# Optimization experiments

Measured on AMD Instinct MI355X. Metric: run time of the kernel, lower is better.

Reference implementation:

```python
import jax, jax.numpy as jnp
import numpy as np

N, E = 50000, 500000          # nodes, edges
IN_DIM, HID, OUT = 512, 256, 64  # hidden_dims = [in_dim, num_hidden, out_dim]


def setup_inputs() -> dict:
    key = jax.random.key(0)
    ks = jax.random.split(key, 6)
    features = jax.random.normal(ks[0], (N, IN_DIM), jnp.float32)
    edge_index = jax.random.randint(ks[1], (2, E), 0, N, jnp.int32)  # [src; dst]
    s1 = 1.0 / np.sqrt(IN_DIM)
    s2 = 1.0 / np.sqrt(HID)
    # torch.nn.Linear convention: weight shape (out, in), y = x @ W.T
    W1 = jax.random.uniform(ks[2], (HID, IN_DIM), jnp.float32, -s1, s1)
    W2 = jax.random.uniform(ks[3], (OUT, HID), jnp.float32, -s2, s2)
    att_src = jax.random.normal(ks[4], (HID,), jnp.float32) * 0.1
    att_dst = jax.random.normal(ks[5], (HID,), jnp.float32) * 0.1
    return dict(features=features, W1=W1, W2=W2,
                att_src=att_src, att_dst=att_dst, edge_index=edge_index)


def _gat_propagate(h, a_src, a_dst, src, dst, n):
    """STAGATE GATConv propagate: sigmoid attention logits + PyG segment softmax
    over destination nodes, then scatter-sum of weighted source features."""
    a = jax.nn.sigmoid(a_src[src] + a_dst[dst])          # [E] edge logits
    mx = jax.ops.segment_max(a, dst, num_segments=n)     # [N] per-dest max
    mx = jnp.where(jnp.isfinite(mx), mx, 0.0)            # empty segments -> 0
    e = jnp.exp(a - mx[dst])                             # [E]
    denom = jax.ops.segment_sum(e, dst, num_segments=n)  # [N]
    w = e / (denom[dst] + 1e-16)                         # [E] softmax weights
    return jax.ops.segment_sum(h[src] * w[:, None], dst, num_segments=n)


def reference(features, W1, W2, att_src, att_dst, edge_index):
    src, dst = edge_index[0], edge_index[1]
    n = features.shape[0]
    # conv1: attention=True (heads=1, concat=False)
    h1p = features @ W1.T                 # [N, HID]
    a_src = h1p @ att_src                 # [N] node-level alpha_src
    a_dst = h1p @ att_dst                 # [N] node-level alpha_dst
    h1 = jax.nn.elu(_gat_propagate(h1p, a_src, a_dst, src, dst, n))
    # conv2: attention=False -> linear only
    h2 = h1 @ W2.T                        # [N, OUT]
    # conv3: weight tied to W2.T, tied_attention = conv1's node alphas
    h3p = h2 @ W2                         # [N, HID]
    h3 = jax.nn.elu(_gat_propagate(h3p, a_src, a_dst, src, dst, n))
    # conv4: attention=False, weight tied to W1.T
    h4 = h3 @ W1                          # [N, IN_DIM]
    return h2, h4
```

## Files before the change

kernel.cpp:

```cpp
#include <hip/hip_runtime.h>
#include <hip/hip_bf16.h>

typedef unsigned short u16;
typedef unsigned int   u32;

#define N_NODES 50000
#define N_EDGES 500000
#define IN_DIM  512
#define HID     256
#define OUT_DIM 64

typedef __bf16 bf16x8 __attribute__((ext_vector_type(8)));
typedef float  f32x4  __attribute__((ext_vector_type(4)));

#define GLOBAL_AS __attribute__((address_space(1)))
#define LDS_AS    __attribute__((address_space(3)))

__device__ __forceinline__ float bf2f(u16 u) {
  union { u32 i; float f; } x; x.i = ((u32)u) << 16; return x.f;
}
__device__ __forceinline__ u16 f2bf(float f) {
  union { float f; u32 i; } x; x.f = f;
  u32 r = x.i + 0x7FFFu + ((x.i >> 16) & 1u);
  return (u16)(r >> 16);
}
__device__ __forceinline__ float lo2f(u32 w) {
  union { u32 i; float f; } x; x.i = w << 16; return x.f;
}
__device__ __forceinline__ float hi2f(u32 w) {
  union { u32 i; float f; } x; x.i = w & 0xFFFF0000u; return x.f;
}

__global__ void detect_dtype(const u32* __restrict__ feat, int* __restrict__ flag) {
  __shared__ int s[256];
  int t = threadIdx.x;
  int hits = 0;
  for (int i = t; i < 1024; i += 256) {
    u32 e = (feat[i] >> 7) & 0xFF;
    hits += (e >= 100 && e <= 140) ? 1 : 0;
  }
  s[t] = hits;
  __syncthreads();
  for (int o = 128; o > 0; o >>= 1) {
    if (t < o) s[t] += s[t + o];
    __syncthreads();
  }
  if (t == 0) *flag = (s[0] > 716) ? 1 : 0;
}

__global__ void cvt8(const void* __restrict__ src, u16* __restrict__ dst, int n8,
                     const int* __restrict__ flag) {
  int i = blockIdx.x * 256 + threadIdx.x;
  if (i >= n8) return;
  if (*flag) {
    ((uint4*)dst)[i] = ((const uint4*)src)[i];
  } else {
    const float4* s4 = (const float4*)src;
    float4 a = s4[2 * i], b = s4[2 * i + 1];
    uint4 o;
    o.x = (u32)f2bf(a.x) | ((u32)f2bf(a.y) << 16);
    o.y = (u32)f2bf(a.z) | ((u32)f2bf(a.w) << 16);
    o.z = (u32)f2bf(b.x) | ((u32)f2bf(b.y) << 16);
    o.w = (u32)f2bf(b.z) | ((u32)f2bf(b.w) << 16);
    ((uint4*)dst)[i] = o;
  }
}

__global__ void transpose_bf16(const u16* __restrict__ src, u16* __restrict__ dst,
                               int R, int C) {
  int i = blockIdx.x * 256 + threadIdx.x;
  if (i < R * C) {
    int r = i / C, c = i - r * C;
    dst[c * R + r] = src[i];
  }
}

__device__ __forceinline__ void glds16(const u16* g, __bf16* l) {
  __builtin_amdgcn_global_load_lds((const GLOBAL_AS u32*)g, (LDS_AS u32*)l, 16, 0, 0);
}

template <int MODE>
__global__ __launch_bounds__(256) void gemm128(const u16* __restrict__ A,
                                               const u16* __restrict__ B,
                                               u16* __restrict__ Cb,
                                               void* __restrict__ outbase,
                                               size_t out_off,
                                               const int* __restrict__ flag,
                                               int M, int N, int K) {
  __shared__ __bf16 As[128 * 32];
  __shared__ __bf16 Bs[128 * 32];

  const int tid  = threadIdx.x;
  const int wave = tid >> 6;
  const int lane = tid & 63;
  const int m0   = blockIdx.x * 128;
  const int n0   = blockIdx.y * 128;
  const int wm   = (wave >> 1) * 64;
  const int wn   = (wave & 1) * 64;
  const int quad = lane >> 4;
  const int l16  = lane & 15;

  const int r_in  = lane >> 2;
  const int s_log = (lane & 3) ^ ((lane >> 3) & 3);
  const int q0 = wave, q1 = wave + 4;
  int ar0 = m0 + q0 * 16 + r_in; if (ar0 >= M) ar0 = M - 1;
  int ar1 = m0 + q1 * 16 + r_in; if (ar1 >= M) ar1 = M - 1;
  const u16* ap0 = A + (size_t)ar0 * K + s_log * 8;
  const u16* ap1 = A + (size_t)ar1 * K + s_log * 8;
  const u16* bp0 = B + (size_t)(n0 + q0 * 16 + r_in) * K + s_log * 8;
  const u16* bp1 = B + (size_t)(n0 + q1 * 16 + r_in) * K + s_log * 8;

  f32x4 acc[4][4];
#pragma unroll
  for (int i = 0; i < 4; ++i)
#pragma unroll
    for (int j = 0; j < 4; ++j) acc[i][j] = (f32x4)0.f;

  const int swz = (l16 >> 1) & 3;

  for (int k0 = 0; k0 < K; k0 += 32) {
    __syncthreads();
    glds16(ap0 + k0, As + q0 * 512);
    glds16(ap1 + k0, As + q1 * 512);
    glds16(bp0 + k0, Bs + q0 * 512);
    glds16(bp1 + k0, Bs + q1 * 512);
    __syncthreads();

    bf16x8 af[4], bfr[4];
#pragma unroll
    for (int mi = 0; mi < 4; ++mi)
      af[mi] = *(const bf16x8*)&As[(wm + mi * 16 + l16) * 32 + ((quad ^ swz) * 8)];
#pragma unroll
    for (int ni = 0; ni < 4; ++ni)
      bfr[ni] = *(const bf16x8*)&Bs[(wn + ni * 16 + l16) * 32 + ((quad ^ swz) * 8)];
#pragma unroll
    for (int mi = 0; mi < 4; ++mi)
#pragma unroll
      for (int ni = 0; ni < 4; ++ni)
        acc[mi][ni] = __builtin_amdgcn_mfma_f32_16x16x32_bf16(
            af[mi], bfr[ni], acc[mi][ni], 0, 0, 0);
  }

  const int out_bf = (MODE == 1) ? *flag : 0;
#pragma unroll
  for (int mi = 0; mi < 4; ++mi)
#pragma unroll
    for (int ni = 0; ni < 4; ++ni)
#pragma unroll
      for (int r = 0; r < 4; ++r) {
        int gr = m0 + wm + mi * 16 + quad * 4 + r;
        int gc = n0 + wn + ni * 16 + l16;
        if (gr < M) {
          float  v   = acc[mi][ni][r];
          size_t idx = (size_t)gr * N + gc;
          if (MODE == 0) {
            Cb[idx] = f2bf(v);
          } else {
            if (out_bf) ((u16*)outbase)[out_off + idx] = f2bf(v);
            else        ((float*)outbase)[out_off + idx] = v;
          }
        }
      }
}

template <int MODE>
__global__ __launch_bounds__(256) void gemm_nt(const u16* __restrict__ A,
                                               const u16* __restrict__ B,
                                               float* __restrict__ Cf,
                                               void* __restrict__ outbase,
                                               size_t out_off,
                                               u16* __restrict__ Cb,
                                               const int* __restrict__ flag,
                                               int M, int N, int K) {
  __shared__ __bf16 As[64 * 48];
  __shared__ __bf16 Bs[64 * 48];

  const int tid  = threadIdx.x;
  const int m0   = blockIdx.x * 64;
  const int n0   = blockIdx.y * 64;
  const int wave = tid >> 6;
  const int lane = tid & 63;
  const int wm   = (wave >> 1) * 32;
  const int wn   = (wave & 1) * 32;
  const int quad = lane >> 4;
  const int l16  = lane & 15;

  const int srow = tid >> 2;
  const int sseg = (tid & 3) * 8;
  int arow = m0 + srow;
  if (arow >= M) arow = M - 1;
  const size_t a_base = (size_t)arow * K + sseg;
  const size_t b_base = (size_t)(n0 + srow) * K + sseg;

  f32x4 acc[2][2];
#pragma unroll
  for (int i = 0; i < 2; ++i)
#pragma unroll
    for (int j = 0; j < 2; ++j) acc[i][j] = (f32x4)0.f;

  for (int k0 = 0; k0 < K; k0 += 32) {
    uint4 av = *(const uint4*)(A + a_base + k0);
    uint4 bv = *(const uint4*)(B + b_base + k0);
    __syncthreads();
    *(uint4*)(&As[srow * 48 + sseg]) = av;
    *(uint4*)(&Bs[srow * 48 + sseg]) = bv;
    __syncthreads();

    bf16x8 af[2], bfr[2];
#pragma unroll
    for (int mi = 0; mi < 2; ++mi)
      af[mi] = *(const bf16x8*)(&As[(wm + mi * 16 + l16) * 48 + quad * 8]);
#pragma unroll
    for (int ni = 0; ni < 2; ++ni)
      bfr[ni] = *(const bf16x8*)(&Bs[(wn + ni * 16 + l16) * 48 + quad * 8]);
#pragma unroll
    for (int mi = 0; mi < 2; ++mi)
#pragma unroll
      for (int ni = 0; ni < 2; ++ni)
        acc[mi][ni] = __builtin_amdgcn_mfma_f32_16x16x32_bf16(
            af[mi], bfr[ni], acc[mi][ni], 0, 0, 0);
  }

  const int out_bf = *flag;
#pragma unroll
  for (int mi = 0; mi < 2; ++mi)
#pragma unroll
    for (int ni = 0; ni < 2; ++ni)
#pragma unroll
      for (int r = 0; r < 4; ++r) {
        int gr = m0 + wm + mi * 16 + quad * 4 + r;
        int gc = n0 + wn + ni * 16 + l16;
        if (gr < M) {
          float  v   = acc[mi][ni][r];
          size_t idx = (size_t)gr * N + gc;
          if (out_bf) ((u16*)outbase)[out_off + idx] = f2bf(v);
          else        ((float*)outbase)[out_off + idx] = v;
          if (MODE == 2) Cb[idx] = f2bf(v);
        }
      }
  (void)Cf;
}

__global__ __launch_bounds__(256) void attn_dots(const u16* __restrict__ h1,
                                                 const u16* __restrict__ atts,
                                                 const u16* __restrict__ attd,
                                                 float* __restrict__ a_s,
                                                 float* __restrict__ a_d) {
  __shared__ __align__(16) float ss[HID];
  __shared__ __align__(16) float sd[HID];
  int t = threadIdx.x;
  ss[t] = bf2f(atts[t]);
  sd[t] = bf2f(attd[t]);
  __syncthreads();
  int row  = blockIdx.x * 4 + (t >> 6);
  int lane = t & 63;
  ushort4 h = ((const ushort4*)(h1 + (size_t)row * HID))[lane];
  float4  s = ((const float4*)ss)[lane];
  float4  d = ((const float4*)sd)[lane];
  float hx = bf2f(h.x), hy = bf2f(h.y), hz = bf2f(h.z), hw = bf2f(h.w);
  float vs = hx * s.x + hy * s.y + hz * s.z + hw * s.w;
  float vd = hx * d.x + hy * d.y + hz * d.z + hw * d.w;
#pragma unroll
  for (int off = 32; off > 0; off >>= 1) {
    vs += __shfl_down(vs, off);
    vd += __shfl_down(vd, off);
  }
  if (lane == 0) {
    a_s[row] = vs;
    a_d[row] = vd;
  }
}

__global__ void hist_kernel(const int* __restrict__ dst, int* __restrict__ counts) {
  int e = blockIdx.x * 256 + threadIdx.x;
  if (e < N_EDGES) atomicAdd(&counts[dst[e]], 1);
}

__global__ void block_sum(const int* __restrict__ counts, int n,
                          int* __restrict__ bsums) {
  __shared__ int s[256];
  int i = blockIdx.x * 256 + threadIdx.x;
  s[threadIdx.x] = (i < n) ? counts[i] : 0;
  __syncthreads();
  for (int off = 128; off > 0; off >>= 1) {
    if (threadIdx.x < off) s[threadIdx.x] += s[threadIdx.x + off];
    __syncthreads();
  }
  if (threadIdx.x == 0) bsums[blockIdx.x] = s[0];
}

__global__ void scan_bsums(const int* __restrict__ bsums, int nb,
                           int* __restrict__ boffs) {
  __shared__ int s[256];
  int t = threadIdx.x;
  int v = (t < nb) ? bsums[t] : 0;
  s[t] = v;
  __syncthreads();
  for (int off = 1; off < 256; off <<= 1) {
    int add = (t >= off) ? s[t - off] : 0;
    __syncthreads();
    s[t] += add;
    __syncthreads();
  }
  boffs[t] = s[t] - v;
}

__global__ void scan_final(const int* __restrict__ counts,
                           const int* __restrict__ boffs, int n,
                           int* __restrict__ offsets, int* __restrict__ cursor) {
  __shared__ int s[256];
  int t = threadIdx.x;
  int i = blockIdx.x * 256 + t;
  int v = (i < n) ? counts[i] : 0;
  s[t] = v;
  __syncthreads();
  for (int off = 1; off < 256; off <<= 1) {
    int add = (t >= off) ? s[t - off] : 0;
    __syncthreads();
    s[t] += add;
    __syncthreads();
  }
  int excl = boffs[blockIdx.x] + s[t] - v;
  if (i < n) {
    offsets[i] = excl;
    cursor[i]  = excl;
  }
  if (i == n - 1) offsets[n] = excl + v;
}

__global__ void edge_scatter(const int* __restrict__ src, const int* __restrict__ dst,
                             const float* __restrict__ a_s, const float* __restrict__ a_d,
                             float* __restrict__ denom, int* __restrict__ cursor,
                             int* __restrict__ csr_src, float* __restrict__ csr_e) {
  int e = blockIdx.x * 256 + threadIdx.x;
  if (e >= N_EDGES) return;
  int s = src[e], d = dst[e];
  float x  = a_s[s] + a_d[d];
  float a  = 1.f / (1.f + expf(-x));
  float ev = expf(a);
  atomicAdd(&denom[d], ev);
  int pos = atomicAdd(&cursor[d], 1);
  csr_src[pos] = s;
  csr_e[pos]   = ev;
}

__global__ __launch_bounds__(256) void propagate_elu8(
    const int* __restrict__ offs, const int* __restrict__ csr_src,
    const float* __restrict__ csr_e, const float* __restrict__ denom,
    const u16* __restrict__ feat, u16* __restrict__ out) {
  const int sub  = threadIdx.x >> 5;
  const int lane = threadIdx.x & 31;
  const int nd   = blockIdx.x * 8 + sub;
  const int col  = lane * 8;
  const int beg = offs[nd], end = offs[nd + 1];
  float a[8];
#pragma unroll
  for (int j = 0; j < 8; ++j) a[j] = 0.f;
  for (int e = beg; e < end; ++e) {
    int   s  = csr_src[e];
    float ev = csr_e[e];
    uint4 w = *(const uint4*)(feat + (size_t)s * HID + col);
    a[0] += ev * lo2f(w.x); a[1] += ev * hi2f(w.x);
    a[2] += ev * lo2f(w.y); a[3] += ev * hi2f(w.y);
    a[4] += ev * lo2f(w.z); a[5] += ev * hi2f(w.z);
    a[6] += ev * lo2f(w.w); a[7] += ev * hi2f(w.w);
  }
  float dn = 1.f / (denom[nd] + 1e-16f);
  uint4 o;
  u32 p[4];
#pragma unroll
  for (int j = 0; j < 4; ++j) {
    float r0 = a[2 * j] * dn;
    float r1 = a[2 * j + 1] * dn;
    r0 = (r0 > 0.f) ? r0 : expm1f(r0);
    r1 = (r1 > 0.f) ? r1 : expm1f(r1);
    p[j] = (u32)f2bf(r0) | ((u32)f2bf(r1) << 16);
  }
  o.x = p[0]; o.y = p[1]; o.z = p[2]; o.w = p[3];
  *(uint4*)(out + (size_t)nd * HID + col) = o;
}

extern "C" void kernel_launch(void* const* d_in, const int* in_sizes, int n_in,
                              void* d_out, int out_size, void* d_ws, size_t ws_size,
                              hipStream_t stream) {
  const void* X    = d_in[0];
  const void* W1   = d_in[1];
  const void* W2   = d_in[2];
  const void* atts = d_in[3];
  const void* attd = d_in[4];
  const int*  eidx = (const int*)d_in[5];
  const int*  esrc = eidx;
  const int*  edst = eidx + N_EDGES;

  char*  ws  = (char*)d_ws;
  size_t off = 0;
  auto alloc = [&](size_t bytes) -> void* {
    void* p = ws + off;
    off += (bytes + 255) & ~(size_t)255;
    return p;
  };
  u16*   Xb     = (u16*)alloc((size_t)N_NODES * IN_DIM * 2);
  u16*   W1b    = (u16*)alloc((size_t)HID * IN_DIM * 2);
  u16*   W2b    = (u16*)alloc((size_t)OUT_DIM * HID * 2);
  u16*   attsb  = (u16*)alloc(HID * 2);
  u16*   attdb  = (u16*)alloc(HID * 2);
  u16*   W1T    = (u16*)alloc((size_t)IN_DIM * HID * 2);
  u16*   W2T    = (u16*)alloc((size_t)HID * OUT_DIM * 2);
  u16*   feat   = (u16*)alloc((size_t)N_NODES * HID * 2);
  u16*   h1     = (u16*)alloc((size_t)N_NODES * HID * 2);
  u16*   h2b    = (u16*)alloc((size_t)N_NODES * OUT_DIM * 2);
  float* a_s    = (float*)alloc(N_NODES * 4);
  float* a_d    = (float*)alloc(N_NODES * 4);
  float* denom  = (float*)alloc(N_NODES * 4);
  int*   counts = (int*)alloc(N_NODES * 4);
  int*   offsets= (int*)alloc((N_NODES + 1) * 4);
  int*   cursor = (int*)alloc(N_NODES * 4);
  int*   bsums  = (int*)alloc(1024 * 4);
  int*   boffs  = (int*)alloc(1024 * 4);
  int*   csrsrc = (int*)alloc((size_t)N_EDGES * 4);
  float* csre   = (float*)alloc((size_t)N_EDGES * 4);
  int*   flag   = (int*)alloc(256);
  (void)ws_size; (void)in_sizes; (void)n_in; (void)out_size;

  size_t zero_bytes = (size_t)((char*)offsets - (char*)denom);
  hipMemsetAsync(denom, 0, zero_bytes, stream);

  detect_dtype<<<1, 256, 0, stream>>>((const u32*)X, flag);

  cvt8<<<(N_NODES * IN_DIM / 8 + 255) / 256, 256, 0, stream>>>(X, Xb, N_NODES * IN_DIM / 8, flag);
  cvt8<<<(HID * IN_DIM / 8 + 255) / 256, 256, 0, stream>>>(W1, W1b, HID * IN_DIM / 8, flag);
  cvt8<<<(OUT_DIM * HID / 8 + 255) / 256, 256, 0, stream>>>(W2, W2b, OUT_DIM * HID / 8, flag);
  cvt8<<<1, 256, 0, stream>>>(atts, attsb, HID / 8, flag);
  cvt8<<<1, 256, 0, stream>>>(attd, attdb, HID / 8, flag);

  transpose_bf16<<<(HID * IN_DIM + 255) / 256, 256, 0, stream>>>(W1b, W1T, HID, IN_DIM);
  transpose_bf16<<<(OUT_DIM * HID + 255) / 256, 256, 0, stream>>>(W2b, W2T, OUT_DIM, HID);

  const int MB128 = (N_NODES + 127) / 128;
  const int MB64  = (N_NODES + 63) / 64;
  gemm128<0><<<dim3(MB128, HID / 128), 256, 0, stream>>>(Xb, W1b, feat, nullptr, 0, flag,
                                                         N_NODES, HID, IN_DIM);
  attn_dots<<<N_NODES / 4, 256, 0, stream>>>(feat, attsb, attdb, a_s, a_d);

  const int NB = (N_NODES + 255) / 256;
  hist_kernel<<<(N_EDGES + 255) / 256, 256, 0, stream>>>(edst, counts);
  block_sum<<<NB, 256, 0, stream>>>(counts, N_NODES, bsums);
  scan_bsums<<<1, 256, 0, stream>>>(bsums, NB, boffs);
  scan_final<<<NB, 256, 0, stream>>>(counts, boffs, N_NODES, offsets, cursor);
  edge_scatter<<<(N_EDGES + 255) / 256, 256, 0, stream>>>(esrc, edst, a_s, a_d,
                                                          denom, cursor, csrsrc, csre);
  propagate_elu8<<<N_NODES / 8, 256, 0, stream>>>(offsets, csrsrc, csre, denom, feat, h1);
  gemm_nt<2><<<dim3(MB64, 1), 256, 0, stream>>>(h1, W2b, nullptr, d_out, 0, h2b, flag,
                                                N_NODES, OUT_DIM, HID);
  gemm128<0><<<dim3(MB128, HID / 128), 256, 0, stream>>>(h2b, W2T, feat, nullptr, 0, flag,
                                                         N_NODES, HID, OUT_DIM);
  propagate_elu8<<<N_NODES / 8, 256, 0, stream>>>(offsets, csrsrc, csre, denom, feat, h1);
  gemm128<1><<<dim3(MB128, IN_DIM / 128), 256, 0, stream>>>(h1, W1T, nullptr, d_out,
                                                            (size_t)N_NODES * OUT_DIM, flag,
                                                            N_NODES, IN_DIM, HID);
}
```

Before: 491.5 us.

## Reorder conv3 propagate before W2 projection, fuse attention dots and conversions

```diff
diff --git a/kernel.cpp b/kernel.cpp
--- a/kernel.cpp
+++ b/kernel.cpp
@@ -48,30 +48,48 @@
   if (t == 0) *flag = (s[0] > 716) ? 1 : 0;
 }
 
-__global__ void cvt8(const void* __restrict__ src, u16* __restrict__ dst, int n8,
-                     const int* __restrict__ flag) {
+__global__ void cvt8_cond(const void* __restrict__ src, u16* __restrict__ dst,
+                          int n8, const int* __restrict__ flag) {
+  if (*flag) return;
   int i = blockIdx.x * 256 + threadIdx.x;
   if (i >= n8) return;
-  if (*flag) {
-    ((uint4*)dst)[i] = ((const uint4*)src)[i];
-  } else {
-    const float4* s4 = (const float4*)src;
-    float4 a = s4[2 * i], b = s4[2 * i + 1];
-    uint4 o;
-    o.x = (u32)f2bf(a.x) | ((u32)f2bf(a.y) << 16);
-    o.y = (u32)f2bf(a.z) | ((u32)f2bf(a.w) << 16);
-    o.z = (u32)f2bf(b.x) | ((u32)f2bf(b.y) << 16);
-    o.w = (u32)f2bf(b.z) | ((u32)f2bf(b.w) << 16);
-    ((uint4*)dst)[i] = o;
-  }
-}
-
-__global__ void transpose_bf16(const u16* __restrict__ src, u16* __restrict__ dst,
-                               int R, int C) {
+  const float4* s4 = (const float4*)src;
+  float4 a = s4[2 * i], b = s4[2 * i + 1];
+  uint4 o;
+  o.x = (u32)f2bf(a.x) | ((u32)f2bf(a.y) << 16);
+  o.y = (u32)f2bf(a.z) | ((u32)f2bf(a.w) << 16);
+  o.z = (u32)f2bf(b.x) | ((u32)f2bf(b.y) << 16);
+  o.w = (u32)f2bf(b.z) | ((u32)f2bf(b.w) << 16);
+  ((uint4*)dst)[i] = o;
+}
+
+__global__ void prep(const void* __restrict__ W1r, const void* __restrict__ W2r,
+                     const void* __restrict__ atsr, const void* __restrict__ atdr,
+                     u16* __restrict__ W1b, u16* __restrict__ W2b,
+                     u16* __restrict__ attsb, u16* __restrict__ attdb,
+                     u16* __restrict__ W1T, u16* __restrict__ W2T,
+                     const int* __restrict__ flag) {
+  const int fv = *flag;
   int i = blockIdx.x * 256 + threadIdx.x;
-  if (i < R * C) {
-    int r = i / C, c = i - r * C;
-    dst[c * R + r] = src[i];
+  int stride = gridDim.x * 256;
+  const int NW1 = HID * IN_DIM;
+  const int NW2 = OUT_DIM * HID;
+  for (int j = i; j < NW1; j += stride) {
+    u16 v = fv ? ((const u16*)W1r)[j] : f2bf(((const float*)W1r)[j]);
+    W1b[j] = v;
+    int r = j >> 9, c = j & 511;
+    W1T[c * HID + r] = v;
+  }
+  for (int j = i; j < NW2; j += stride) {
+    u16 v = fv ? ((const u16*)W2r)[j] : f2bf(((const float*)W2r)[j]);
+    W2b[j] = v;
+    int r = j >> 8, c = j & 255;
+    W2T[c * OUT_DIM + r] = v;
+  }
+  if (blockIdx.x == 0 && threadIdx.x < HID) {
+    int t = threadIdx.x;
+    attsb[t] = fv ? ((const u16*)atsr)[t] : f2bf(((const float*)atsr)[t]);
+    attdb[t] = fv ? ((const u16*)atdr)[t] : f2bf(((const float*)atdr)[t]);
   }
 }
 
@@ -81,14 +99,24 @@
 
 template <int MODE>
 __global__ __launch_bounds__(256) void gemm128(const u16* __restrict__ A,
+                                               const u16* __restrict__ Aalt,
                                                const u16* __restrict__ B,
                                                u16* __restrict__ Cb,
                                                void* __restrict__ outbase,
                                                size_t out_off,
+                                               const u16* __restrict__ attsb,
+                                               const u16* __restrict__ attdb,
+                                               float* __restrict__ a_s,
+                                               float* __restrict__ a_d,
                                                const int* __restrict__ flag,
                                                int M, int N, int K) {
   __shared__ __bf16 As[128 * 32];
   __shared__ __bf16 Bs[128 * 32];
+  __shared__ float as_l[128];
+  __shared__ float ad_l[128];
+
+  const int fv = *flag;
+  if (Aalt && fv) A = Aalt;
 
   const int tid  = threadIdx.x;
   const int wave = tid >> 6;
@@ -100,6 +128,11 @@
   const int quad = lane >> 4;
   const int l16  = lane & 15;
 
+  if (MODE == 3 && tid < 128) {
+    as_l[tid] = bf2f(attsb[n0 + tid]);
+    ad_l[tid] = bf2f(attdb[n0 + tid]);
+  }
+
   const int r_in  = lane >> 2;
   const int s_log = (lane & 3) ^ ((lane >> 3) & 3);
   const int q0 = wave, q1 = wave + 4;
@@ -141,7 +174,32 @@
             af[mi], bfr[ni], acc[mi][ni], 0, 0, 0);
   }
 
-  const int out_bf = (MODE == 1) ? *flag : 0;
+  if (MODE == 3) {
+    __syncthreads();
+#pragma unroll
+    for (int mi = 0; mi < 4; ++mi)
+#pragma unroll
+      for (int r = 0; r < 4; ++r) {
+        float ps = 0.f, pd = 0.f;
+#pragma unroll
+        for (int ni = 0; ni < 4; ++ni) {
+          int c = wn + ni * 16 + l16;
+          ps += acc[mi][ni][r] * as_l[c];
+          pd += acc[mi][ni][r] * ad_l[c];
+        }
+#pragma unroll
+        for (int o = 1; o < 16; o <<= 1) {
+          ps += __shfl_xor(ps, o);
+          pd += __shfl_xor(pd, o);
+        }
+        int gr = m0 + wm + mi * 16 + quad * 4 + r;
+        if (l16 == 0 && gr < M) {
+          atomicAdd(&a_s[gr], ps);
+          atomicAdd(&a_d[gr], pd);
+        }
+      }
+  }
+
 #pragma unroll
   for (int mi = 0; mi < 4; ++mi)
 #pragma unroll
@@ -153,22 +211,22 @@
         if (gr < M) {
           float  v   = acc[mi][ni][r];
           size_t idx = (size_t)gr * N + gc;
-          if (MODE == 0) {
+          if (MODE == 1) {
+            if (fv) ((u16*)outbase)[out_off + idx] = f2bf(v);
+            else    ((float*)outbase)[out_off + idx] = v;
+          } else if (MODE == 2) {
+            v = (v > 0.f) ? v : expm1f(v);
             Cb[idx] = f2bf(v);
           } else {
-            if (out_bf) ((u16*)outbase)[out_off + idx] = f2bf(v);
-            else        ((float*)outbase)[out_off + idx] = v;
+            Cb[idx] = f2bf(v);
           }
         }
       }
 }
 
-template <int MODE>
-__global__ __launch_bounds__(256) void gemm_nt(const u16* __restrict__ A,
+__global__ __launch_bounds__(256) void gemm_h2(const u16* __restrict__ A,
                                                const u16* __restrict__ B,
-                                               float* __restrict__ Cf,
                                                void* __restrict__ outbase,
-                                               size_t out_off,
                                                u16* __restrict__ Cb,
                                                const int* __restrict__ flag,
                                                int M, int N, int K) {
@@ -177,7 +235,6 @@
 
   const int tid  = threadIdx.x;
   const int m0   = blockIdx.x * 64;
-  const int n0   = blockIdx.y * 64;
   const int wave = tid >> 6;
   const int lane = tid & 63;
   const int wm   = (wave >> 1) * 32;
@@ -190,7 +247,7 @@
   int arow = m0 + srow;
   if (arow >= M) arow = M - 1;
   const size_t a_base = (size_t)arow * K + sseg;
-  const size_t b_base = (size_t)(n0 + srow) * K + sseg;
+  const size_t b_base = (size_t)srow * K + sseg;
 
   f32x4 acc[2][2];
 #pragma unroll
@@ -221,7 +278,7 @@
             af[mi], bfr[ni], acc[mi][ni], 0, 0, 0);
   }
 
-  const int out_bf = *flag;
+  const int fv = *flag;
 #pragma unroll
   for (int mi = 0; mi < 2; ++mi)
 #pragma unroll
@@ -229,46 +286,16 @@
 #pragma unroll
       for (int r = 0; r < 4; ++r) {
         int gr = m0 + wm + mi * 16 + quad * 4 + r;
-        int gc = n0 + wn + ni * 16 + l16;
-        if (gr < M) {
+        int gc = wn + ni * 16 + l16;
+        if (gr < M && gc < N) {
           float  v   = acc[mi][ni][r];
           size_t idx = (size_t)gr * N + gc;
-          if (out_bf) ((u16*)outbase)[out_off + idx] = f2bf(v);
-          else        ((float*)outbase)[out_off + idx] = v;
-          if (MODE == 2) Cb[idx] = f2bf(v);
+          u16 bv = f2bf(v);
+          if (fv) ((u16*)outbase)[idx] = bv;
+          else    ((float*)outbase)[idx] = v;
+          Cb[idx] = bv;
         }
       }
-  (void)Cf;
-}
-
-__global__ __launch_bounds__(256) void attn_dots(const u16* __restrict__ h1,
-                                                 const u16* __restrict__ atts,
-                                                 const u16* __restrict__ attd,
-                                                 float* __restrict__ a_s,
-                                                 float* __restrict__ a_d) {
-  __shared__ __align__(16) float ss[HID];
-  __shared__ __align__(16) float sd[HID];
-  int t = threadIdx.x;
-  ss[t] = bf2f(atts[t]);
-  sd[t] = bf2f(attd[t]);
-  __syncthreads();
-  int row  = blockIdx.x * 4 + (t >> 6);
-  int lane = t & 63;
-  ushort4 h = ((const ushort4*)(h1 + (size_t)row * HID))[lane];
-  float4  s = ((const float4*)ss)[lane];
-  float4  d = ((const float4*)sd)[lane];
-  float hx = bf2f(h.x), hy = bf2f(h.y), hz = bf2f(h.z), hw = bf2f(h.w);
-  float vs = hx * s.x + hy * s.y + hz * s.z + hw * s.w;
-  float vd = hx * d.x + hy * d.y + hz * d.z + hw * d.w;
-#pragma unroll
-  for (int off = 32; off > 0; off >>= 1) {
-    vs += __shfl_down(vs, off);
-    vd += __shfl_down(vd, off);
-  }
-  if (lane == 0) {
-    a_s[row] = vs;
-    a_d[row] = vd;
-  }
 }
 
 __global__ void hist_kernel(const int* __restrict__ dst, int* __restrict__ counts) {
@@ -331,7 +358,7 @@
 __global__ void edge_scatter(const int* __restrict__ src, const int* __restrict__ dst,
                              const float* __restrict__ a_s, const float* __restrict__ a_d,
                              float* __restrict__ denom, int* __restrict__ cursor,
-                             int* __restrict__ csr_src, float* __restrict__ csr_e) {
+                             int2* __restrict__ edges) {
   int e = blockIdx.x * 256 + threadIdx.x;
   if (e >= N_EDGES) return;
   int s = src[e], d = dst[e];
@@ -340,14 +367,13 @@
   float ev = expf(a);
   atomicAdd(&denom[d], ev);
   int pos = atomicAdd(&cursor[d], 1);
-  csr_src[pos] = s;
-  csr_e[pos]   = ev;
-}
-
-__global__ __launch_bounds__(256) void propagate_elu8(
-    const int* __restrict__ offs, const int* __restrict__ csr_src,
-    const float* __restrict__ csr_e, const float* __restrict__ denom,
-    const u16* __restrict__ feat, u16* __restrict__ out) {
+  edges[pos] = make_int2(s, __float_as_int(ev));
+}
+
+__global__ __launch_bounds__(256) void prop256(
+    const int* __restrict__ offs, const int2* __restrict__ edges,
+    const float* __restrict__ denom, const u16* __restrict__ feat,
+    u16* __restrict__ out) {
   const int sub  = threadIdx.x >> 5;
   const int lane = threadIdx.x & 31;
   const int nd   = blockIdx.x * 8 + sub;
@@ -357,16 +383,15 @@
 #pragma unroll
   for (int j = 0; j < 8; ++j) a[j] = 0.f;
   for (int e = beg; e < end; ++e) {
-    int   s  = csr_src[e];
-    float ev = csr_e[e];
-    uint4 w = *(const uint4*)(feat + (size_t)s * HID + col);
+    int2  ed = edges[e];
+    float ev = __int_as_float(ed.y);
+    uint4 w = *(const uint4*)(feat + (size_t)ed.x * HID + col);
     a[0] += ev * lo2f(w.x); a[1] += ev * hi2f(w.x);
     a[2] += ev * lo2f(w.y); a[3] += ev * hi2f(w.y);
     a[4] += ev * lo2f(w.z); a[5] += ev * hi2f(w.z);
     a[6] += ev * lo2f(w.w); a[7] += ev * hi2f(w.w);
   }
   float dn = 1.f / (denom[nd] + 1e-16f);
-  uint4 o;
   u32 p[4];
 #pragma unroll
   for (int j = 0; j < 4; ++j) {
@@ -376,8 +401,38 @@
     r1 = (r1 > 0.f) ? r1 : expm1f(r1);
     p[j] = (u32)f2bf(r0) | ((u32)f2bf(r1) << 16);
   }
-  o.x = p[0]; o.y = p[1]; o.z = p[2]; o.w = p[3];
-  *(uint4*)(out + (size_t)nd * HID + col) = o;
+  *(uint4*)(out + (size_t)nd * HID + col) = make_uint4(p[0], p[1], p[2], p[3]);
+}
+
+__global__ __launch_bounds__(256) void prop64(
+    const int* __restrict__ offs, const int2* __restrict__ edges,
+    const float* __restrict__ denom, const u16* __restrict__ feat,
+    u16* __restrict__ out) {
+  const int sub  = threadIdx.x >> 3;
+  const int lane = threadIdx.x & 7;
+  const int nd   = blockIdx.x * 32 + sub;
+  if (nd >= N_NODES) return;
+  const int col  = lane * 8;
+  const int beg = offs[nd], end = offs[nd + 1];
+  float a[8];
+#pragma unroll
+  for (int j = 0; j < 8; ++j) a[j] = 0.f;
+  for (int e = beg; e < end; ++e) {
+    int2  ed = edges[e];
+    float ev = __int_as_float(ed.y);
+    uint4 w = *(const uint4*)(feat + (size_t)ed.x * OUT_DIM + col);
+    a[0] += ev * lo2f(w.x); a[1] += ev * hi2f(w.x);
+    a[2] += ev * lo2f(w.y); a[3] += ev * hi2f(w.y);
+    a[4] += ev * lo2f(w.z); a[5] += ev * hi2f(w.z);
+    a[6] += ev * lo2f(w.w); a[7] += ev * hi2f(w.w);
+  }
+  float dn = 1.f / (denom[nd] + 1e-16f);
+  u32 p[4];
+#pragma unroll
+  for (int j = 0; j < 4; ++j) {
+    p[j] = (u32)f2bf(a[2 * j] * dn) | ((u32)f2bf(a[2 * j + 1] * dn) << 16);
+  }
+  *(uint4*)(out + (size_t)nd * OUT_DIM + col) = make_uint4(p[0], p[1], p[2], p[3]);
 }
 
 extern "C" void kernel_launch(void* const* d_in, const int* in_sizes, int n_in,
@@ -409,6 +464,7 @@
   u16*   feat   = (u16*)alloc((size_t)N_NODES * HID * 2);
   u16*   h1     = (u16*)alloc((size_t)N_NODES * HID * 2);
   u16*   h2b    = (u16*)alloc((size_t)N_NODES * OUT_DIM * 2);
+  u16*   ph2    = (u16*)alloc((size_t)N_NODES * OUT_DIM * 2);
   float* a_s    = (float*)alloc(N_NODES * 4);
   float* a_d    = (float*)alloc(N_NODES * 4);
   float* denom  = (float*)alloc(N_NODES * 4);
@@ -417,30 +473,25 @@
   int*   cursor = (int*)alloc(N_NODES * 4);
   int*   bsums  = (int*)alloc(1024 * 4);
   int*   boffs  = (int*)alloc(1024 * 4);
-  int*   csrsrc = (int*)alloc((size_t)N_EDGES * 4);
-  float* csre   = (float*)alloc((size_t)N_EDGES * 4);
+  int2*  edges  = (int2*)alloc((size_t)N_EDGES * 8);
   int*   flag   = (int*)alloc(256);
   (void)ws_size; (void)in_sizes; (void)n_in; (void)out_size;
 
-  size_t zero_bytes = (size_t)((char*)offsets - (char*)denom);
-  hipMemsetAsync(denom, 0, zero_bytes, stream);
+  size_t zero_bytes = (size_t)((char*)offsets - (char*)a_s);
+  hipMemsetAsync(a_s, 0, zero_bytes, stream);
 
   detect_dtype<<<1, 256, 0, stream>>>((const u32*)X, flag);
-
-  cvt8<<<(N_NODES * IN_DIM / 8 + 255) / 256, 256, 0, stream>>>(X, Xb, N_NODES * IN_DIM / 8, flag);
-  cvt8<<<(HID * IN_DIM / 8 + 255) / 256, 256, 0, stream>>>(W1, W1b, HID * IN_DIM / 8, flag);
-  cvt8<<<(OUT_DIM * HID / 8 + 255) / 256, 256, 0, stream>>>(W2, W2b, OUT_DIM * HID / 8, flag);
-  cvt8<<<1, 256, 0, stream>>>(atts, attsb, HID / 8, flag);
-  cvt8<<<1, 256, 0, stream>>>(attd, attdb, HID / 8, flag);
-
-  transpose_bf16<<<(HID * IN_DIM + 255) / 256, 256, 0, stream>>>(W1b, W1T, HID, IN_DIM);
-  transpose_bf16<<<(OUT_DIM * HID + 255) / 256, 256, 0, stream>>>(W2b, W2T, OUT_DIM, HID);
+  cvt8_cond<<<(N_NODES * IN_DIM / 8 + 255) / 256, 256, 0, stream>>>(
+      X, Xb, N_NODES * IN_DIM / 8, flag);
+  prep<<<512, 256, 0, stream>>>(W1, W2, atts, attd, W1b, W2b, attsb, attdb,
+                                W1T, W2T, flag);
 
   const int MB128 = (N_NODES + 127) / 128;
   const int MB64  = (N_NODES + 63) / 64;
-  gemm128<0><<<dim3(MB128, HID / 128), 256, 0, stream>>>(Xb, W1b, feat, nullptr, 0, flag,
-                                                         N_NODES, HID, IN_DIM);
-  attn_dots<<<N_NODES / 4, 256, 0, stream>>>(feat, attsb, attdb, a_s, a_d);
+
+  gemm128<3><<<dim3(MB128, HID / 128), 256, 0, stream>>>(
+      Xb, (const u16*)X, W1b, feat, nullptr, 0, attsb, attdb, a_s, a_d, flag,
+      N_NODES, HID, IN_DIM);
 
   const int NB = (N_NODES + 255) / 256;
   hist_kernel<<<(N_EDGES + 255) / 256, 256, 0, stream>>>(edst, counts);
@@ -448,14 +499,16 @@
   scan_bsums<<<1, 256, 0, stream>>>(bsums, NB, boffs);
   scan_final<<<NB, 256, 0, stream>>>(counts, boffs, N_NODES, offsets, cursor);
   edge_scatter<<<(N_EDGES + 255) / 256, 256, 0, stream>>>(esrc, edst, a_s, a_d,
-                                                          denom, cursor, csrsrc, csre);
-  propagate_elu8<<<N_NODES / 8, 256, 0, stream>>>(offsets, csrsrc, csre, denom, feat, h1);
-  gemm_nt<2><<<dim3(MB64, 1), 256, 0, stream>>>(h1, W2b, nullptr, d_out, 0, h2b, flag,
-                                                N_NODES, OUT_DIM, HID);
-  gemm128<0><<<dim3(MB128, HID / 128), 256, 0, stream>>>(h2b, W2T, feat, nullptr, 0, flag,
-                                                         N_NODES, HID, OUT_DIM);
-  propagate_elu8<<<N_NODES / 8, 256, 0, stream>>>(offsets, csrsrc, csre, denom, feat, h1);
-  gemm128<1><<<dim3(MB128, IN_DIM / 128), 256, 0, stream>>>(h1, W1T, nullptr, d_out,
-                                                            (size_t)N_NODES * OUT_DIM, flag,
-                                                            N_NODES, IN_DIM, HID);
-}
+                                                          denom, cursor, edges);
+
+  prop256<<<N_NODES / 8, 256, 0, stream>>>(offsets, edges, denom, feat, h1);
+  gemm_h2<<<dim3(MB64, 1), 256, 0, stream>>>(h1, W2b, d_out, h2b, flag,
+                                             N_NODES, OUT_DIM, HID);
+  prop64<<<(N_NODES + 31) / 32, 256, 0, stream>>>(offsets, edges, denom, h2b, ph2);
+  gemm128<2><<<dim3(MB128, HID / 128), 256, 0, stream>>>(
+      ph2, nullptr, W2T, feat, nullptr, 0, nullptr, nullptr, nullptr, nullptr, flag,
+      N_NODES, HID, OUT_DIM);
+  gemm128<1><<<dim3(MB128, IN_DIM / 128), 256, 0, stream>>>(
+      feat, nullptr, W1T, nullptr, d_out, (size_t)N_NODES * OUT_DIM,
+      nullptr, nullptr, nullptr, nullptr, flag, N_NODES, IN_DIM, HID);
+}
```

New measurement: 461.6 us. 1.06x faster.
